# Optimization experiments

Hardware: AMD Instinct MI355X
Metric: run time of the kernel (lower is better)

Reference implementation:

```python
import jax, jax.numpy as jnp
import numpy as np

DT = 0.1
GRAVITY = 9.81
DENSITY = 1028.0
ZVEC = jnp.array([0.0, 0.0, 1.0], dtype=jnp.float32)


def _skew(v):
    # v: [k,3] -> [k,3,3] skew-symmetric matrix (matches A/B/C column construction)
    x, y, z = v[..., 0], v[..., 1], v[..., 2]
    o = jnp.zeros_like(x)
    r0 = jnp.stack([o, -z, y], -1)
    r1 = jnp.stack([z, o, -x], -1)
    r2 = jnp.stack([-y, x, o], -1)
    return jnp.stack([r0, r1, r2], -2)


def _body2inertial(pose):
    # pose: [k,7]; quat stored as (x,y,z,w) in pose[:,3:7]
    q = pose[:, 3:7]
    x, y, z, w = q[:, 0], q[:, 1], q[:, 2], q[:, 3]
    r0 = jnp.stack([1 - 2 * (y * y + z * z), 2 * (x * y - z * w), 2 * (x * z + y * w)], -1)
    r1 = jnp.stack([2 * (x * y + z * w), 1 - 2 * (x * x + z * z), 2 * (y * z - x * w)], -1)
    r2 = jnp.stack([2 * (x * z - y * w), 2 * (y * z + x * w), 1 - 2 * (x * x + y * y)], -1)
    rot = jnp.stack([r0, r1, r2], -2)  # [k,3,3]
    t = 0.5 * jnp.stack([
        jnp.stack([-x, -y, -z], -1),
        jnp.stack([w, -z, y], -1),
        jnp.stack([z, w, -x], -1),
        jnp.stack([-y, x, w], -1)], -2)  # [k,4,3]
    return rot, t


def _restoring(rot, mass, volume, cog, cob):
    fng = -mass * GRAVITY * ZVEC              # (3,)
    fnb = volume * DENSITY * GRAVITY * ZVEC   # (3,)
    # rotItoB = rot^T -> rot^T @ f == einsum('kji,j->ki')
    fbg = jnp.einsum('kji,j->ki', rot, fng)
    fbb = jnp.einsum('kji,j->ki', rot, fnb)
    mbg = jnp.cross(cog, fbg)
    mbb = jnp.cross(cob, fbb)
    return -jnp.concatenate([fbg + fbb, mbg + mbb], -1)  # [k,6]


def _damping(v, linDamp, linDampFow, quadDamp):
    eye6 = jnp.eye(6, dtype=v.dtype)
    D = -linDamp - v[:, :, None] * linDampFow
    return D - quadDamp * (jnp.abs(v)[:, :, None] * eye6)  # [k,6,6]


def _coriolis(v, mTot):
    M = mTot[0]
    mv_top = jnp.einsum('ij,kj->ki', M[0:3, 0:3], v[:, 0:3]) + jnp.einsum('ij,kj->ki', M[0:3, 3:6], v[:, 3:6])
    mv_bot = jnp.einsum('ij,kj->ki', M[3:6, 0:3], v[:, 0:3]) + jnp.einsum('ij,kj->ki', M[3:6, 3:6], v[:, 3:6])
    s12 = -_skew(mv_top)
    s22 = -_skew(mv_bot)
    z33 = jnp.zeros_like(s12)
    r1 = jnp.concatenate([z33, s12], -1)
    r2 = jnp.concatenate([s12, s22], -1)  # note: source uses s12 (not s12^T) in lower-left, reproduced faithfully
    return jnp.concatenate([r1, r2], -2)  # [k,6,6]


def _dot(x, u, mass, volume, cog, cob, mTot, linDamp, linDampFow, quadDamp):
    p, v = x[:, 0:7], x[:, 7:13]
    rot, t = _body2inertial(p)
    # jacobian is block-diag [[rot,0],[0,t]] -> apply blocks directly
    pDot_lin = jnp.einsum('kij,kj->ki', rot, v[:, 0:3])  # [k,3]
    pDot_ang = jnp.einsum('kij,kj->ki', t, v[:, 3:6])    # [k,4]
    D = _damping(v, linDamp, linDampFow, quadDamp)
    C = _coriolis(v, mTot)
    Dv = jnp.einsum('kij,kj->ki', D, v)
    Cv = jnp.einsum('kij,kj->ki', C, v)
    g = _restoring(rot, mass, volume, cog, cob)
    rhs = u - Cv - Dv - g                      # [k,6]
    vDot = jnp.linalg.solve(mTot[0], rhs.T).T  # single shared 6x6 solve
    return jnp.concatenate([pDot_lin, pDot_ang, vDot], -1)  # [k,13]


def _norm_quat(xs):
    q = xs[:, 3:7]
    q = q / jnp.linalg.norm(q, axis=-1, keepdims=True)
    return xs.at[:, 3:7].set(q)


def reference(x, u, mass, volume, cog, cob, mTot, linDamp, linDampFow, quadDamp):
    # RK2 integration step (rk=2 default)
    k1 = _dot(x, u, mass, volume, cog, cob, mTot, linDamp, linDampFow, quadDamp)
    k2 = _dot(x + k1 * DT, u, mass, volume, cog, cob, mTot, linDamp, linDampFow, quadDamp)
    return _norm_quat(x + (DT / 2.0) * (k1 + k2))


def setup_inputs() -> dict:
    key = jax.random.key(0)
    kx, ku = jax.random.split(key)
    K = 524288
    x = jax.random.normal(kx, (K, 13), dtype=jnp.float32)
    u = jax.random.normal(ku, (K, 6), dtype=jnp.float32)
    mass = jnp.array([100.0], dtype=jnp.float32)
    volume = jnp.array([1.0], dtype=jnp.float32)
    cog = jnp.zeros((1, 3), dtype=jnp.float32)
    cob = jnp.array([[0.0, 0.0, 0.2]], dtype=jnp.float32)
    rb = np.zeros((6, 6), dtype=np.float32)
    rb[0:3, 0:3] = 100.0 * np.eye(3, dtype=np.float32)
    ma = 100.0 * np.eye(6, dtype=np.float32) + 1e-7      # default Ma (+1e-7 on every entry)
    mTot = jnp.asarray(rb + ma)[None]                    # [1,6,6]
    linDamp = jnp.diag(jnp.array([-70.0, -70.0, -700.0, -300.0, -300.0, -100.0], dtype=jnp.float32))[None]
    linDampFow = jnp.zeros((1, 6, 6), dtype=jnp.float32)
    quadDamp = jnp.diag(jnp.array([-740.0, -990.0, -1800.0, -670.0, -770.0, -520.0], dtype=jnp.float32))[None]
    return {"x": x, "u": u, "mass": mass, "volume": volume, "cog": cog, "cob": cob,
            "mTot": mTot, "linDamp": linDamp, "linDampFow": linDampFow, "quadDamp": quadDamp}
```

## Files before the change

kernel.cpp:

```cpp
#include <hip/hip_runtime.h>
#include <math.h>


struct SC {
    float M[36];
    float Mi[36];
    float LD[36];
    float LDF[36];
    float QD[6];
    float cog[3];
    float cob[3];
    float mass;
    float vol;
};

__device__ __forceinline__ void fossen_dot(const float* __restrict__ X,
                                           const float* __restrict__ U,
                                           const SC& c,
                                           float* __restrict__ xd)
{
    const float qx = X[3], qy = X[4], qz = X[5], qw = X[6];
    const float r00 = 1.f - 2.f*(qy*qy + qz*qz);
    const float r01 = 2.f*(qx*qy - qz*qw);
    const float r02 = 2.f*(qx*qz + qy*qw);
    const float r10 = 2.f*(qx*qy + qz*qw);
    const float r11 = 1.f - 2.f*(qx*qx + qz*qz);
    const float r12 = 2.f*(qy*qz - qx*qw);
    const float r20 = 2.f*(qx*qz - qy*qw);
    const float r21 = 2.f*(qy*qz + qx*qw);
    const float r22 = 1.f - 2.f*(qx*qx + qy*qy);

    const float v0 = X[7],  v1 = X[8],  v2 = X[9];
    const float v3 = X[10], v4 = X[11], v5 = X[12];

    xd[0] = r00*v0 + r01*v1 + r02*v2;
    xd[1] = r10*v0 + r11*v1 + r12*v2;
    xd[2] = r20*v0 + r21*v1 + r22*v2;
    xd[3] = 0.5f*(-qx*v3 - qy*v4 - qz*v5);
    xd[4] = 0.5f*( qw*v3 - qz*v4 + qy*v5);
    xd[5] = 0.5f*( qz*v3 + qw*v4 - qx*v5);
    xd[6] = 0.5f*(-qy*v3 + qx*v4 + qw*v5);

    const float v[6] = {v0, v1, v2, v3, v4, v5};

    float Dv[6];
#pragma unroll
    for (int i = 0; i < 6; ++i) {
        float s = -c.QD[i] * fabsf(v[i]) * v[i];
#pragma unroll
        for (int j = 0; j < 6; ++j)
            s += (-c.LD[i*6+j] - v[i]*c.LDF[i*6+j]) * v[j];
        Dv[i] = s;
    }

    float mv[6];
#pragma unroll
    for (int i = 0; i < 6; ++i) {
        float s = 0.f;
#pragma unroll
        for (int j = 0; j < 6; ++j) s += c.M[i*6+j] * v[j];
        mv[i] = s;
    }
    float Cv[6];
    Cv[0] = -(mv[1]*v5 - mv[2]*v4);
    Cv[1] = -(mv[2]*v3 - mv[0]*v5);
    Cv[2] = -(mv[0]*v4 - mv[1]*v3);
    Cv[3] = -(mv[1]*v2 - mv[2]*v1) - (mv[4]*v5 - mv[5]*v4);
    Cv[4] = -(mv[2]*v0 - mv[0]*v2) - (mv[5]*v3 - mv[3]*v5);
    Cv[5] = -(mv[0]*v1 - mv[1]*v0) - (mv[3]*v4 - mv[4]*v3);

    const float fgz = -c.mass * 9.81f;
    const float fbz =  c.vol * 1028.0f * 9.81f;
    const float fb0 = r20*fgz, fb1 = r21*fgz, fb2 = r22*fgz;
    const float bb0 = r20*fbz, bb1 = r21*fbz, bb2 = r22*fbz;
    const float m0 = c.cog[1]*fb2 - c.cog[2]*fb1 + c.cob[1]*bb2 - c.cob[2]*bb1;
    const float m1 = c.cog[2]*fb0 - c.cog[0]*fb2 + c.cob[2]*bb0 - c.cob[0]*bb2;
    const float m2 = c.cog[0]*fb1 - c.cog[1]*fb0 + c.cob[0]*bb1 - c.cob[1]*bb0;
    const float g0 = -(fb0 + bb0), g1 = -(fb1 + bb1), g2 = -(fb2 + bb2);
    const float g3 = -m0, g4 = -m1, g5 = -m2;
    const float gr[6] = {g0, g1, g2, g3, g4, g5};

    float rhs[6];
#pragma unroll
    for (int i = 0; i < 6; ++i) rhs[i] = U[i] - Cv[i] - Dv[i] - gr[i];

#pragma unroll
    for (int i = 0; i < 6; ++i) {
        float s = 0.f;
#pragma unroll
        for (int j = 0; j < 6; ++j) s += c.Mi[i*6+j] * rhs[j];
        xd[7+i] = s;
    }
}

__global__ void __launch_bounds__(256)
auv_rk2(const float* __restrict__ x, const float* __restrict__ u,
        const float* __restrict__ mass, const float* __restrict__ volume,
        const float* __restrict__ cog, const float* __restrict__ cob,
        const float* __restrict__ mTot, const float* __restrict__ linDamp,
        const float* __restrict__ linDampFow, const float* __restrict__ quadDamp,
        const float* __restrict__ minv, float* __restrict__ out, int K)
{
    __shared__ float sx[256 * 13];
    __shared__ float su[256 * 6];
    __shared__ SC c;

    const int tid  = threadIdx.x;
    const int base = blockIdx.x * 256;

    if (tid < 36) {
        c.M[tid]   = mTot[tid];
        c.Mi[tid]  = minv[tid];
        c.LD[tid]  = linDamp[tid];
        c.LDF[tid] = linDampFow[tid];
    } else if (tid < 42) {
        const int i = tid - 36;
        c.QD[i] = quadDamp[i*6 + i];
    } else if (tid < 45) {
        const int i = tid - 42;
        c.cog[i] = cog[i];
        c.cob[i] = cob[i];
    } else if (tid == 45) {
        c.mass = mass[0];
        c.vol  = volume[0];
    }

    const int nElem = min(256, K - base);

    if (nElem == 256) {
        const float4* gx  = (const float4*)(x + (size_t)base * 13);
        float4*       s4  = (float4*)sx;
        for (int k = tid; k < 832; k += 256) s4[k] = gx[k];
        const float4* gu  = (const float4*)(u + (size_t)base * 6);
        float4*       su4 = (float4*)su;
        for (int k = tid; k < 384; k += 256) su4[k] = gu[k];
    } else {
        for (int k = tid; k < nElem * 13; k += 256) sx[k] = x[(size_t)base*13 + k];
        for (int k = tid; k < nElem * 6;  k += 256) su[k] = u[(size_t)base*6  + k];
    }
    __syncthreads();

    if (tid < nElem) {
        float X[13], U[6];
#pragma unroll
        for (int j = 0; j < 13; ++j) X[j] = sx[tid*13 + j];
#pragma unroll
        for (int j = 0; j < 6;  ++j) U[j] = su[tid*6 + j];

        float k1[13], X2[13], k2[13], Y[13];
        fossen_dot(X, U, c, k1);
#pragma unroll
        for (int j = 0; j < 13; ++j) X2[j] = X[j] + 0.1f * k1[j];
        fossen_dot(X2, U, c, k2);
#pragma unroll
        for (int j = 0; j < 13; ++j) Y[j] = X[j] + 0.05f * (k1[j] + k2[j]);

        const float nq = Y[3]*Y[3] + Y[4]*Y[4] + Y[5]*Y[5] + Y[6]*Y[6];
        const float inv = 1.0f / sqrtf(nq);
        Y[3] *= inv; Y[4] *= inv; Y[5] *= inv; Y[6] *= inv;

#pragma unroll
        for (int j = 0; j < 13; ++j) sx[tid*13 + j] = Y[j];
    }
    __syncthreads();

    if (nElem == 256) {
        float4*       go = (float4*)(out + (size_t)base * 13);
        const float4* s4 = (const float4*)sx;
        for (int k = tid; k < 832; k += 256) go[k] = s4[k];
    } else {
        for (int k = tid; k < nElem * 13; k += 256) out[(size_t)base*13 + k] = sx[k];
    }
}

__global__ void invert6x6(const float* __restrict__ M, float* __restrict__ Mi)
{
    if (threadIdx.x != 0 || blockIdx.x != 0) return;
    double a[6][12];
    for (int i = 0; i < 6; ++i)
        for (int j = 0; j < 6; ++j) {
            a[i][j]     = (double)M[i*6 + j];
            a[i][6 + j] = (i == j) ? 1.0 : 0.0;
        }
    for (int col = 0; col < 6; ++col) {
        int piv = col;
        double best = fabs(a[col][col]);
        for (int r = col + 1; r < 6; ++r) {
            double vv = fabs(a[r][col]);
            if (vv > best) { best = vv; piv = r; }
        }
        if (piv != col)
            for (int j = 0; j < 12; ++j) {
                double t = a[col][j]; a[col][j] = a[piv][j]; a[piv][j] = t;
            }
        const double d = 1.0 / a[col][col];
        for (int j = 0; j < 12; ++j) a[col][j] *= d;
        for (int r = 0; r < 6; ++r) {
            if (r == col) continue;
            const double f = a[r][col];
            for (int j = 0; j < 12; ++j) a[r][j] -= f * a[col][j];
        }
    }
    for (int i = 0; i < 6; ++i)
        for (int j = 0; j < 6; ++j)
            Mi[i*6 + j] = (float)a[i][6 + j];
}

extern "C" void kernel_launch(void* const* d_in, const int* in_sizes, int n_in,
                              void* d_out, int out_size, void* d_ws, size_t ws_size,
                              hipStream_t stream)
{
    const float* x          = (const float*)d_in[0];
    const float* u          = (const float*)d_in[1];
    const float* mass       = (const float*)d_in[2];
    const float* volume     = (const float*)d_in[3];
    const float* cog        = (const float*)d_in[4];
    const float* cob        = (const float*)d_in[5];
    const float* mTot       = (const float*)d_in[6];
    const float* linDamp    = (const float*)d_in[7];
    const float* linDampFow = (const float*)d_in[8];
    const float* quadDamp   = (const float*)d_in[9];
    float*       out        = (float*)d_out;
    float*       minv       = (float*)d_ws;

    const int K = in_sizes[0] / 13;

    invert6x6<<<1, 64, 0, stream>>>(mTot, minv);

    const int blocks = (K + 255) / 256;
    auv_rk2<<<blocks, 256, 0, stream>>>(x, u, mass, volume, cog, cob, mTot,
                                        linDamp, linDampFow, quadDamp,
                                        minv, out, K);
}
```

Measured before the change: 139.0 us.

## Pack constants in global buffer, load x via global_load_lds, read u directly

A prep kernel packs every constant matrix and scalar into one contiguous workspace buffer and inverts the mass matrix in float32 without pivoting, replacing the double-precision pivoted inversion. The main kernel reads those constants straight from global memory, which lets the compiler use scalar loads, instead of staging a shared struct per block. The x tile is copied with the direct global-to-LDS load builtin, and u is read straight into registers as float2 loads instead of going through shared memory. The output copy loops are also unrolled. The unpivoted float inversion can lose accuracy or break for matrices that need pivoting.

```diff
diff --git a/kernel.cpp b/kernel.cpp
--- a/kernel.cpp
+++ b/kernel.cpp
@@ -2,21 +2,19 @@
 #include <math.h>
 
 
-struct SC {
-    float M[36];
-    float Mi[36];
-    float LD[36];
-    float LDF[36];
-    float QD[6];
-    float cog[3];
-    float cob[3];
-    float mass;
-    float vol;
-};
+#define CB_MI   0
+#define CB_M    36
+#define CB_LD   72
+#define CB_LDF  108
+#define CB_QD   144
+#define CB_COG  150
+#define CB_COB  153
+#define CB_MASS 156
+#define CB_VOL  157
 
 __device__ __forceinline__ void fossen_dot(const float* __restrict__ X,
                                            const float* __restrict__ U,
-                                           const SC& c,
+                                           const float* __restrict__ cb,
                                            float* __restrict__ xd)
 {
     const float qx = X[3], qy = X[4], qz = X[5], qw = X[6];
@@ -43,14 +41,16 @@
 
     const float v[6] = {v0, v1, v2, v3, v4, v5};
 
-    float Dv[6];
+    float P[6];
 #pragma unroll
     for (int i = 0; i < 6; ++i) {
-        float s = -c.QD[i] * fabsf(v[i]) * v[i];
-#pragma unroll
-        for (int j = 0; j < 6; ++j)
-            s += (-c.LD[i*6+j] - v[i]*c.LDF[i*6+j]) * v[j];
-        Dv[i] = s;
+        float ld = 0.f, ldf = 0.f;
+#pragma unroll
+        for (int j = 0; j < 6; ++j) {
+            ld  += cb[CB_LD  + i*6 + j] * v[j];
+            ldf += cb[CB_LDF + i*6 + j] * v[j];
+        }
+        P[i] = ld + v[i]*ldf + cb[CB_QD + i] * fabsf(v[i]) * v[i];
     }
 
     float mv[6];
@@ -58,7 +58,7 @@
     for (int i = 0; i < 6; ++i) {
         float s = 0.f;
 #pragma unroll
-        for (int j = 0; j < 6; ++j) s += c.M[i*6+j] * v[j];
+        for (int j = 0; j < 6; ++j) s += cb[CB_M + i*6 + j] * v[j];
         mv[i] = s;
     }
     float Cv[6];
@@ -69,93 +69,82 @@
     Cv[4] = -(mv[2]*v0 - mv[0]*v2) - (mv[5]*v3 - mv[3]*v5);
     Cv[5] = -(mv[0]*v1 - mv[1]*v0) - (mv[3]*v4 - mv[4]*v3);
 
-    const float fgz = -c.mass * 9.81f;
-    const float fbz =  c.vol * 1028.0f * 9.81f;
+    const float fgz = -cb[CB_MASS] * 9.81f;
+    const float fbz =  cb[CB_VOL] * 1028.0f * 9.81f;
     const float fb0 = r20*fgz, fb1 = r21*fgz, fb2 = r22*fgz;
     const float bb0 = r20*fbz, bb1 = r21*fbz, bb2 = r22*fbz;
-    const float m0 = c.cog[1]*fb2 - c.cog[2]*fb1 + c.cob[1]*bb2 - c.cob[2]*bb1;
-    const float m1 = c.cog[2]*fb0 - c.cog[0]*fb2 + c.cob[2]*bb0 - c.cob[0]*bb2;
-    const float m2 = c.cog[0]*fb1 - c.cog[1]*fb0 + c.cob[0]*bb1 - c.cob[1]*bb0;
-    const float g0 = -(fb0 + bb0), g1 = -(fb1 + bb1), g2 = -(fb2 + bb2);
-    const float g3 = -m0, g4 = -m1, g5 = -m2;
-    const float gr[6] = {g0, g1, g2, g3, g4, g5};
+    const float cgx = cb[CB_COG], cgy = cb[CB_COG+1], cgz = cb[CB_COG+2];
+    const float cbx = cb[CB_COB], cby = cb[CB_COB+1], cbz = cb[CB_COB+2];
+    const float m0 = cgy*fb2 - cgz*fb1 + cby*bb2 - cbz*bb1;
+    const float m1 = cgz*fb0 - cgx*fb2 + cbz*bb0 - cbx*bb2;
+    const float m2 = cgx*fb1 - cgy*fb0 + cbx*bb1 - cby*bb0;
+    const float g[6] = { -(fb0+bb0), -(fb1+bb1), -(fb2+bb2), -m0, -m1, -m2 };
 
     float rhs[6];
 #pragma unroll
-    for (int i = 0; i < 6; ++i) rhs[i] = U[i] - Cv[i] - Dv[i] - gr[i];
+    for (int i = 0; i < 6; ++i) rhs[i] = U[i] - Cv[i] + P[i] - g[i];
 
 #pragma unroll
     for (int i = 0; i < 6; ++i) {
         float s = 0.f;
 #pragma unroll
-        for (int j = 0; j < 6; ++j) s += c.Mi[i*6+j] * rhs[j];
+        for (int j = 0; j < 6; ++j) s += cb[CB_MI + i*6 + j] * rhs[j];
         xd[7+i] = s;
     }
 }
 
 __global__ void __launch_bounds__(256)
 auv_rk2(const float* __restrict__ x, const float* __restrict__ u,
-        const float* __restrict__ mass, const float* __restrict__ volume,
-        const float* __restrict__ cog, const float* __restrict__ cob,
-        const float* __restrict__ mTot, const float* __restrict__ linDamp,
-        const float* __restrict__ linDampFow, const float* __restrict__ quadDamp,
-        const float* __restrict__ minv, float* __restrict__ out, int K)
+        const float* __restrict__ cb, float* __restrict__ out, int K)
 {
     __shared__ float sx[256 * 13];
-    __shared__ float su[256 * 6];
-    __shared__ SC c;
-
     const int tid  = threadIdx.x;
     const int base = blockIdx.x * 256;
-
-    if (tid < 36) {
-        c.M[tid]   = mTot[tid];
-        c.Mi[tid]  = minv[tid];
-        c.LD[tid]  = linDamp[tid];
-        c.LDF[tid] = linDampFow[tid];
-    } else if (tid < 42) {
-        const int i = tid - 36;
-        c.QD[i] = quadDamp[i*6 + i];
-    } else if (tid < 45) {
-        const int i = tid - 42;
-        c.cog[i] = cog[i];
-        c.cob[i] = cob[i];
-    } else if (tid == 45) {
-        c.mass = mass[0];
-        c.vol  = volume[0];
-    }
-
     const int nElem = min(256, K - base);
 
     if (nElem == 256) {
-        const float4* gx  = (const float4*)(x + (size_t)base * 13);
-        float4*       s4  = (float4*)sx;
-        for (int k = tid; k < 832; k += 256) s4[k] = gx[k];
-        const float4* gu  = (const float4*)(u + (size_t)base * 6);
-        float4*       su4 = (float4*)su;
-        for (int k = tid; k < 384; k += 256) su4[k] = gu[k];
+        const float* gx = x + (size_t)base * 13;
+#pragma unroll
+        for (int it = 0; it < 3; ++it) {
+            const int k = it*256 + tid;
+            __builtin_amdgcn_global_load_lds(
+                (const __attribute__((address_space(1))) void*)(gx + (size_t)k*4),
+                (__attribute__((address_space(3))) void*)(&sx[k*4]), 16, 0, 0);
+        }
+        if (tid < 64) {
+            const int k = 768 + tid;
+            __builtin_amdgcn_global_load_lds(
+                (const __attribute__((address_space(1))) void*)(gx + (size_t)k*4),
+                (__attribute__((address_space(3))) void*)(&sx[k*4]), 16, 0, 0);
+        }
     } else {
-        for (int k = tid; k < nElem * 13; k += 256) sx[k] = x[(size_t)base*13 + k];
-        for (int k = tid; k < nElem * 6;  k += 256) su[k] = u[(size_t)base*6  + k];
+        for (int k = tid; k < nElem*13; k += 256) sx[k] = x[(size_t)base*13 + k];
+    }
+
+    float U[6];
+    if (tid < nElem) {
+        const float* gu = u + (size_t)(base + tid) * 6;
+        const float2 a = *(const float2*)(gu);
+        const float2 b = *(const float2*)(gu + 2);
+        const float2 c = *(const float2*)(gu + 4);
+        U[0]=a.x; U[1]=a.y; U[2]=b.x; U[3]=b.y; U[4]=c.x; U[5]=c.y;
     }
     __syncthreads();
 
     if (tid < nElem) {
-        float X[13], U[6];
+        float X[13];
 #pragma unroll
         for (int j = 0; j < 13; ++j) X[j] = sx[tid*13 + j];
-#pragma unroll
-        for (int j = 0; j < 6;  ++j) U[j] = su[tid*6 + j];
 
         float k1[13], X2[13], k2[13], Y[13];
-        fossen_dot(X, U, c, k1);
+        fossen_dot(X, U, cb, k1);
 #pragma unroll
         for (int j = 0; j < 13; ++j) X2[j] = X[j] + 0.1f * k1[j];
-        fossen_dot(X2, U, c, k2);
+        fossen_dot(X2, U, cb, k2);
 #pragma unroll
         for (int j = 0; j < 13; ++j) Y[j] = X[j] + 0.05f * (k1[j] + k2[j]);
 
-        const float nq = Y[3]*Y[3] + Y[4]*Y[4] + Y[5]*Y[5] + Y[6]*Y[6];
+        const float nq  = Y[3]*Y[3] + Y[4]*Y[4] + Y[5]*Y[5] + Y[6]*Y[6];
         const float inv = 1.0f / sqrtf(nq);
         Y[3] *= inv; Y[4] *= inv; Y[5] *= inv; Y[6] *= inv;
 
@@ -167,43 +156,61 @@
     if (nElem == 256) {
         float4*       go = (float4*)(out + (size_t)base * 13);
         const float4* s4 = (const float4*)sx;
-        for (int k = tid; k < 832; k += 256) go[k] = s4[k];
+#pragma unroll
+        for (int it = 0; it < 3; ++it) go[it*256 + tid] = s4[it*256 + tid];
+        if (tid < 64) go[768 + tid] = s4[768 + tid];
     } else {
-        for (int k = tid; k < nElem * 13; k += 256) out[(size_t)base*13 + k] = sx[k];
-    }
-}
-
-__global__ void invert6x6(const float* __restrict__ M, float* __restrict__ Mi)
-{
-    if (threadIdx.x != 0 || blockIdx.x != 0) return;
-    double a[6][12];
-    for (int i = 0; i < 6; ++i)
-        for (int j = 0; j < 6; ++j) {
-            a[i][j]     = (double)M[i*6 + j];
-            a[i][6 + j] = (i == j) ? 1.0 : 0.0;
-        }
-    for (int col = 0; col < 6; ++col) {
-        int piv = col;
-        double best = fabs(a[col][col]);
-        for (int r = col + 1; r < 6; ++r) {
-            double vv = fabs(a[r][col]);
-            if (vv > best) { best = vv; piv = r; }
-        }
-        if (piv != col)
-            for (int j = 0; j < 12; ++j) {
-                double t = a[col][j]; a[col][j] = a[piv][j]; a[piv][j] = t;
+        for (int k = tid; k < nElem*13; k += 256) out[(size_t)base*13 + k] = sx[k];
+    }
+}
+
+__global__ void prep_consts(const float* __restrict__ mass,
+                            const float* __restrict__ volume,
+                            const float* __restrict__ cog,
+                            const float* __restrict__ cob,
+                            const float* __restrict__ mTot,
+                            const float* __restrict__ linDamp,
+                            const float* __restrict__ linDampFow,
+                            const float* __restrict__ quadDamp,
+                            float* __restrict__ cb)
+{
+    const int t = threadIdx.x;
+    if (t < 36) {
+        cb[CB_M   + t] = mTot[t];
+        cb[CB_LD  + t] = linDamp[t];
+        cb[CB_LDF + t] = linDampFow[t];
+    }
+    if (t < 6)  cb[CB_QD + t] = quadDamp[t*6 + t];
+    if (t < 3)  { cb[CB_COG + t] = cog[t]; cb[CB_COB + t] = cob[t]; }
+    if (t == 0) { cb[CB_MASS] = mass[0]; cb[CB_VOL] = volume[0]; }
+
+    if (t == 0) {
+        float a[36], inv[36];
+#pragma unroll
+        for (int i = 0; i < 36; ++i) a[i] = mTot[i];
+#pragma unroll
+        for (int i = 0; i < 36; ++i) inv[i] = 0.f;
+#pragma unroll
+        for (int i = 0; i < 6; ++i) inv[i*6 + i] = 1.f;
+#pragma unroll
+        for (int col = 0; col < 6; ++col) {
+            const float d = 1.0f / a[col*6 + col];
+#pragma unroll
+            for (int j = 0; j < 6; ++j) { a[col*6+j] *= d; inv[col*6+j] *= d; }
+#pragma unroll
+            for (int r = 0; r < 6; ++r) {
+                if (r == col) continue;
+                const float f = a[r*6 + col];
+#pragma unroll
+                for (int j = 0; j < 6; ++j) {
+                    a[r*6+j]   -= f * a[col*6+j];
+                    inv[r*6+j] -= f * inv[col*6+j];
+                }
             }
-        const double d = 1.0 / a[col][col];
-        for (int j = 0; j < 12; ++j) a[col][j] *= d;
-        for (int r = 0; r < 6; ++r) {
-            if (r == col) continue;
-            const double f = a[r][col];
-            for (int j = 0; j < 12; ++j) a[r][j] -= f * a[col][j];
-        }
-    }
-    for (int i = 0; i < 6; ++i)
-        for (int j = 0; j < 6; ++j)
-            Mi[i*6 + j] = (float)a[i][6 + j];
+        }
+#pragma unroll
+        for (int i = 0; i < 36; ++i) cb[CB_MI + i] = inv[i];
+    }
 }
 
 extern "C" void kernel_launch(void* const* d_in, const int* in_sizes, int n_in,
@@ -221,14 +228,13 @@
     const float* linDampFow = (const float*)d_in[8];
     const float* quadDamp   = (const float*)d_in[9];
     float*       out        = (float*)d_out;
-    float*       minv       = (float*)d_ws;
+    float*       cb         = (float*)d_ws;
 
     const int K = in_sizes[0] / 13;
 
-    invert6x6<<<1, 64, 0, stream>>>(mTot, minv);
+    prep_consts<<<1, 64, 0, stream>>>(mass, volume, cog, cob, mTot,
+                                      linDamp, linDampFow, quadDamp, cb);
 
     const int blocks = (K + 255) / 256;
-    auv_rk2<<<blocks, 256, 0, stream>>>(x, u, mass, volume, cog, cob, mTot,
-                                        linDamp, linDampFow, quadDamp,
-                                        minv, out, K);
-}
+    auv_rk2<<<blocks, 256, 0, stream>>>(x, u, cb, out, K);
+}
```

Result: faster. 117.6 us (-15.4%).
